# Performance work log

Measured on AMD Instinct MI355X. Metric: run time of the kernel, lower is better.

The kernel has to match this reference:

```python
import jax, jax.numpy as jnp
import numpy as np

K_LAYERS = 10
ALPHA = 0.1
N_NODES = 100000
N_EDGES = 500000
N_PATHS = 3
D = 128
HID = 128


def setup_inputs() -> dict:
    key = jax.random.key(0)
    k1, k2, k3, k4 = jax.random.split(key, 4)
    h = jax.random.normal(k1, (N_NODES, D), dtype=jnp.float32)
    edges = jax.random.randint(k2, (N_PATHS, 2, N_EDGES), 0, N_NODES, dtype=jnp.int64)
    W1 = jax.random.normal(k3, (D, HID), dtype=jnp.float32) * (1.0 / np.sqrt(D))
    b1 = jnp.zeros((HID,), dtype=jnp.float32)
    w2 = jax.random.normal(k4, (HID, 1), dtype=jnp.float32) * (1.0 / np.sqrt(HID))
    return {"h": h, "edges": edges, "W1": W1, "b1": b1, "w2": w2}


def _appnp(h0, src, dst):
    # DGL APPNPConv (eval mode, no dropout): symmetric degree normalization,
    # K steps of h <- (1-alpha) * D_in^{-1/2} A D_out^{-1/2} h + alpha * h0
    n = h0.shape[0]
    ones = jnp.ones(src.shape[0], dtype=h0.dtype)
    out_deg = jnp.clip(jax.ops.segment_sum(ones, src, num_segments=n), 1.0)
    in_deg = jnp.clip(jax.ops.segment_sum(ones, dst, num_segments=n), 1.0)
    norm_s = out_deg ** -0.5  # [N]
    norm_d = in_deg ** -0.5   # [N]

    def step(x, _):
        msg = (x * norm_s[:, None])[src]                       # [E, D] gather
        agg = jax.ops.segment_sum(msg, dst, num_segments=n)    # [N, D] scatter-add
        x = (1.0 - ALPHA) * (agg * norm_d[:, None]) + ALPHA * h0
        return x, None

    x, _ = jax.lax.scan(step, h0, None, length=K_LAYERS)
    return x


def reference(h, edges, W1, b1, w2):
    src = edges[:, 0, :]  # [P, E]
    dst = edges[:, 1, :]
    # one APPNP propagation per meta-path, vmapped over the P axis
    z = jax.vmap(lambda s, d: _appnp(h, s, d))(src, dst)  # [P, N, D]
    z = jnp.transpose(z, (1, 0, 2))                        # [N, P, D]
    # semantic attention: small MLP -> mean over nodes -> softmax over paths
    w = jnp.tanh(z @ W1 + b1) @ w2   # [N, P, 1]
    w = w.mean(axis=0)               # [P, 1]
    beta = jax.nn.softmax(w, axis=0) # [P, 1]
    return (beta[None, :, :] * z).sum(axis=1)  # [N, D]
```

## Files before the change

kernel.cpp:

```cpp
#include <hip/hip_runtime.h>
#include <math.h>

#define N_NODES 100000
#define N_EDGES 500000
#define N_PATHS 3
#define DIM 128
#define K_LAYERS 10
#define NBLK_PER_PATH ((N_NODES + 255) / 256)
#define PN (N_PATHS * N_NODES)
#define HRANGE 16384
#define NRANGE ((N_NODES + HRANGE - 1) / HRANGE)
#define BPG 8

typedef __attribute__((ext_vector_type(8))) short bf16x8;
typedef __attribute__((ext_vector_type(4))) float f32x4;

__device__ __forceinline__ float bflo(unsigned u) { return __uint_as_float(u << 16); }
__device__ __forceinline__ float bfhi(unsigned u) { return __uint_as_float(u & 0xffff0000u); }

__global__ __launch_bounds__(256) void hist_kernel(const int* __restrict__ edges,
                                                   int* __restrict__ partial) {
    __shared__ int hist[HRANGE];
    int g = blockIdx.x / BPG;
    int b = blockIdx.x - g * BPG;
    int r = g % NRANGE;
    int pt = g / NRANGE;
    int p = pt >> 1, t = pt & 1;
    for (int i = threadIdx.x; i < HRANGE; i += 256) hist[i] = 0;
    __syncthreads();
    const int* arr = edges + ((size_t)p * 2 + t) * N_EDGES;
    int lo = r * HRANGE;
    const int chunk = N_EDGES / BPG;
    int beg = b * chunk;
    for (int i = beg + threadIdx.x; i < beg + chunk; i += 256) {
        int v = arr[i] - lo;
        if ((unsigned)v < HRANGE) atomicAdd(&hist[v], 1);
    }
    __syncthreads();
    int* outp = partial + ((size_t)g * BPG + b) * HRANGE;
    for (int i = threadIdx.x; i < HRANGE; i += 256) outp[i] = hist[i];
}

__global__ __launch_bounds__(256) void deg_reduce_kernel(const int* __restrict__ partial,
                                                         float* __restrict__ norm_s,
                                                         float* __restrict__ norm_d,
                                                         int* __restrict__ degD_tot) {
    int i = blockIdx.x * 256 + threadIdx.x;
    if (i >= PN) return;
    int p = i / N_NODES, n = i - p * N_NODES;
    int r = n / HRANGE, off = n - r * HRANGE;
    const int* ps = partial + (((size_t)(p * 2 + 0) * NRANGE + r) * BPG) * HRANGE + off;
    const int* pd = partial + (((size_t)(p * 2 + 1) * NRANGE + r) * BPG) * HRANGE + off;
    int sS = 0, sD = 0;
#pragma unroll
    for (int b = 0; b < BPG; ++b) {
        sS += ps[(size_t)b * HRANGE];
        sD += pd[(size_t)b * HRANGE];
    }
    norm_s[i] = 1.0f / sqrtf(fmaxf((float)sS, 1.0f));
    norm_d[i] = 1.0f / sqrtf(fmaxf((float)sD, 1.0f));
    degD_tot[i] = sD;
}

__global__ __launch_bounds__(256) void blocksum_kernel(const int* __restrict__ cnt,
                                                       int* __restrict__ bsum) {
    int b = blockIdx.x;
    int p = b / NBLK_PER_PATH;
    int lb = b - p * NBLK_PER_PATH;
    int idx = lb * 256 + threadIdx.x;
    int v = (idx < N_NODES) ? cnt[p * N_NODES + idx] : 0;
#pragma unroll
    for (int off = 32; off; off >>= 1) v += __shfl_xor(v, off);
    __shared__ int ws[4];
    if ((threadIdx.x & 63) == 0) ws[threadIdx.x >> 6] = v;
    __syncthreads();
    if (threadIdx.x == 0) bsum[b] = ws[0] + ws[1] + ws[2] + ws[3];
}

__global__ __launch_bounds__(512) void bscan_kernel(int* __restrict__ bsum) {
    __shared__ int s[512];
    int p = blockIdx.x;
    int t = threadIdx.x;
    int v = (t < NBLK_PER_PATH) ? bsum[p * NBLK_PER_PATH + t] : 0;
    s[t] = v;
    __syncthreads();
    for (int off = 1; off < 512; off <<= 1) {
        int x = s[t];
        int a = (t >= off) ? s[t - off] : 0;
        __syncthreads();
        s[t] = x + a;
        __syncthreads();
    }
    if (t < NBLK_PER_PATH) bsum[p * NBLK_PER_PATH + t] = s[t] - v;
}

__global__ __launch_bounds__(256) void scan_write_kernel(const int* __restrict__ cnt,
                                                         const int* __restrict__ bsum,
                                                         int* __restrict__ row_ptr_all,
                                                         int* __restrict__ cursor_all) {
    __shared__ int s[256];
    int b = blockIdx.x;
    int p = b / NBLK_PER_PATH;
    int lb = b - p * NBLK_PER_PATH;
    int idx = lb * 256 + threadIdx.x;
    int t = threadIdx.x;
    int v = (idx < N_NODES) ? cnt[p * N_NODES + idx] : 0;
    s[t] = v;
    __syncthreads();
    for (int off = 1; off < 256; off <<= 1) {
        int x = s[t];
        int a = (t >= off) ? s[t - off] : 0;
        __syncthreads();
        s[t] = x + a;
        __syncthreads();
    }
    int excl = s[t] - v + bsum[b];
    if (idx < N_NODES) {
        row_ptr_all[p * (N_NODES + 1) + idx] = excl;
        cursor_all[p * N_NODES + idx] = excl;
        if (idx == N_NODES - 1)
            row_ptr_all[p * (N_NODES + 1) + N_NODES] = excl + v;
    }
}

__global__ __launch_bounds__(256) void fill_kernel(const int* __restrict__ edges,
                                                   const float* __restrict__ norm_s,
                                                   const float* __restrict__ norm_d,
                                                   int* __restrict__ cursor,
                                                   int2* __restrict__ cw) {
    int idx = blockIdx.x * 256 + threadIdx.x;
    if (idx < N_PATHS * N_EDGES) {
        int p = idx / N_EDGES;
        int e = idx - p * N_EDGES;
        const int* src = edges + (size_t)p * 2 * N_EDGES;
        const int* dst = src + N_EDGES;
        int s = src[e], d = dst[e];
        int pos = atomicAdd(&cursor[p * N_NODES + d], 1);
        float w = 0.9f * norm_s[p * N_NODES + s] * norm_d[p * N_NODES + d];
        cw[(size_t)p * N_EDGES + pos] = make_int2(s, __float_as_int(w));
    }
}

__device__ __forceinline__ unsigned bf16pack(float a, float b) {
    unsigned ua = __float_as_uint(a), ub = __float_as_uint(b);
    ua = (ua + 0x7fffu + ((ua >> 16) & 1)) >> 16;
    ub = (ub + 0x7fffu + ((ub >> 16) & 1)) >> 16;
    return ua | (ub << 16);
}

__global__ __launch_bounds__(256) void cast_kernel(const float4* __restrict__ in,
                                                   ushort4* __restrict__ outp) {
    int idx = blockIdx.x * 256 + threadIdx.x;
    if (idx < N_NODES * DIM / 4) {
        float4 v = in[idx];
        ushort4 o;
        unsigned u;
        u = __float_as_uint(v.x); o.x = (unsigned short)((u + 0x7fff + ((u >> 16) & 1)) >> 16);
        u = __float_as_uint(v.y); o.y = (unsigned short)((u + 0x7fff + ((u >> 16) & 1)) >> 16);
        u = __float_as_uint(v.z); o.z = (unsigned short)((u + 0x7fff + ((u >> 16) & 1)) >> 16);
        u = __float_as_uint(v.w); o.w = (unsigned short)((u + 0x7fff + ((u >> 16) & 1)) >> 16);
        outp[idx] = o;
    }
}

__global__ __launch_bounds__(256) void w1t_kernel(const float* __restrict__ W1,
                                                  unsigned short* __restrict__ W1t) {
    int idx = blockIdx.x * 256 + threadIdx.x;
    if (idx < DIM * DIM) {
        int c = idx >> 7, k = idx & 127;
        unsigned u = __float_as_uint(W1[k * DIM + c]);
        W1t[idx] = (unsigned short)((u + 0x7fff + ((u >> 16) & 1)) >> 16);
    }
}

template <int OUT_F32, int H_BF16>
__global__ __launch_bounds__(256) void prop_kernel(const unsigned short* __restrict__ xin,
                                                   size_t in_stride,
                                                   const void* __restrict__ anchor,
                                                   void* __restrict__ xout,
                                                   const int* __restrict__ row_ptr,
                                                   const int2* __restrict__ cw) {
    int wid  = threadIdx.x >> 6;
    int lane = threadIdx.x & 63;
    int q    = lane >> 4;
    int ql   = lane & 15;
    int nodeBase = blockIdx.x * 16 + wid * 4;
    int p  = nodeBase / N_NODES;
    int nb = nodeBase - p * N_NODES;
    const int*  rp   = row_ptr + p * (N_NODES + 1);
    const int2* cwp  = cw + (size_t)p * N_EDGES;
    const uint4* xin4 = (const uint4*)(xin + (size_t)p * in_stride);

    int rv = 0;
    if (lane < 5) rv = rp[nb + lane];
    int beg = __shfl(rv, q);
    int end = __shfl(rv, q + 1);
    int deg = end - beg;
    int myNode = nb + q;
    int maxd = deg;
    maxd = max(maxd, __shfl_xor(maxd, 16));
    maxd = max(maxd, __shfl_xor(maxd, 32));

    float a0 = 0.f, a1 = 0.f, a2 = 0.f, a3 = 0.f;
    float a4 = 0.f, a5 = 0.f, a6 = 0.f, a7 = 0.f;

    for (int base = 0; base < maxd; base += 16) {
        int2 e = make_int2(0, 0);
        if (base + ql < deg) e = cwp[beg + base + ql];
        int lim = maxd - base; if (lim > 16) lim = 16;
#pragma unroll 4
        for (int j = 0; j < lim; ++j) {
            int lsrc = (lane & 48) | j;
            int   c = __shfl(e.x, lsrc);
            float w = __int_as_float(__shfl(e.y, lsrc));
            if (base + j < deg) {
                uint4 v = xin4[(size_t)c * 16 + ql];
                a0 = fmaf(w, bflo(v.x), a0);
                a1 = fmaf(w, bfhi(v.x), a1);
                a2 = fmaf(w, bflo(v.y), a2);
                a3 = fmaf(w, bfhi(v.y), a3);
                a4 = fmaf(w, bflo(v.z), a4);
                a5 = fmaf(w, bfhi(v.z), a5);
                a6 = fmaf(w, bflo(v.w), a6);
                a7 = fmaf(w, bfhi(v.w), a7);
            }
        }
    }

    if (H_BF16) {
        uint4 hv = ((const uint4*)anchor)[(size_t)myNode * 16 + ql];
        a0 += 0.1f * bflo(hv.x); a1 += 0.1f * bfhi(hv.x);
        a2 += 0.1f * bflo(hv.y); a3 += 0.1f * bfhi(hv.y);
        a4 += 0.1f * bflo(hv.z); a5 += 0.1f * bfhi(hv.z);
        a6 += 0.1f * bflo(hv.w); a7 += 0.1f * bfhi(hv.w);
    } else {
        const float4* h4 = (const float4*)anchor + (size_t)myNode * 32;
        float4 h0v = h4[ql * 2];
        float4 h1v = h4[ql * 2 + 1];
        a0 += 0.1f * h0v.x; a1 += 0.1f * h0v.y; a2 += 0.1f * h0v.z; a3 += 0.1f * h0v.w;
        a4 += 0.1f * h1v.x; a5 += 0.1f * h1v.y; a6 += 0.1f * h1v.z; a7 += 0.1f * h1v.w;
    }

    size_t row = (size_t)p * N_NODES + myNode;
    if (OUT_F32) {
        float4* zo = (float4*)xout + row * 32;
        zo[ql * 2]     = make_float4(a0, a1, a2, a3);
        zo[ql * 2 + 1] = make_float4(a4, a5, a6, a7);
    } else {
        uint4 o;
        o.x = bf16pack(a0, a1);
        o.y = bf16pack(a2, a3);
        o.z = bf16pack(a4, a5);
        o.w = bf16pack(a6, a7);
        ((uint4*)xout)[row * 16 + ql] = o;
    }
}

__device__ __forceinline__ float fast_tanh(float x) {
    float e = __expf(2.0f * x);
    return 1.0f - 2.0f / (e + 1.0f);
}

__global__ __launch_bounds__(256) void attn_kernel(const float* __restrict__ z,
                                                   const unsigned short* __restrict__ W1t,
                                                   const float* __restrict__ b1,
                                                   const float* __restrict__ w2,
                                                   float* __restrict__ wsum) {
    const int wid  = threadIdx.x >> 6;
    const int lane = threadIdx.x & 63;
    const int c0   = lane & 15;
    const int kh   = lane >> 4;

    const bf16x8* w1t8 = (const bf16x8*)W1t;
    bf16x8 Bf[8][4];
#pragma unroll
    for (int nt = 0; nt < 8; ++nt)
#pragma unroll
        for (int ks = 0; ks < 4; ++ks)
            Bf[nt][ks] = w1t8[(nt * 16 + c0) * 16 + ks * 4 + kh];

    float b1v[8], w2v[8];
#pragma unroll
    for (int nt = 0; nt < 8; ++nt) {
        b1v[nt] = b1[nt * 16 + c0];
        w2v[nt] = w2[nt * 16 + c0];
    }

    float accP0 = 0.f, accP1 = 0.f, accP2 = 0.f;
    const int NTILES = N_PATHS * N_NODES / 16;
    const int TPP    = N_NODES / 16;
    const int stride = gridDim.x * 4;
    const float4* zf4 = (const float4*)z;

    for (int t = blockIdx.x * 4 + wid; t < NTILES; t += stride) {
        size_t rbase = ((size_t)t * 16 + c0) * 32 + kh * 2;
        bf16x8 Af[4];
#pragma unroll
        for (int ks = 0; ks < 4; ++ks) {
            float4 x0 = zf4[rbase + ks * 8];
            float4 x1 = zf4[rbase + ks * 8 + 1];
            union { uint4 u; bf16x8 v; } cv;
            cv.u.x = bf16pack(x0.x, x0.y);
            cv.u.y = bf16pack(x0.z, x0.w);
            cv.u.z = bf16pack(x1.x, x1.y);
            cv.u.w = bf16pack(x1.z, x1.w);
            Af[ks] = cv.v;
        }
        f32x4 acc[8];
#pragma unroll
        for (int nt = 0; nt < 8; ++nt) acc[nt] = (f32x4){0.f, 0.f, 0.f, 0.f};
#pragma unroll
        for (int nt = 0; nt < 8; ++nt)
#pragma unroll
            for (int ks = 0; ks < 4; ++ks)
                acc[nt] = __builtin_amdgcn_mfma_f32_16x16x32_bf16(Af[ks], Bf[nt][ks], acc[nt], 0, 0, 0);

        float psum = 0.f;
#pragma unroll
        for (int nt = 0; nt < 8; ++nt) {
            psum += fast_tanh(acc[nt][0] + b1v[nt]) * w2v[nt];
            psum += fast_tanh(acc[nt][1] + b1v[nt]) * w2v[nt];
            psum += fast_tanh(acc[nt][2] + b1v[nt]) * w2v[nt];
            psum += fast_tanh(acc[nt][3] + b1v[nt]) * w2v[nt];
        }
#pragma unroll
        for (int off = 32; off; off >>= 1) psum += __shfl_xor(psum, off);
        if (lane == 0) {
            int p = t / TPP;
            if (p == 0) accP0 += psum;
            else if (p == 1) accP1 += psum;
            else accP2 += psum;
        }
    }
    if (lane == 0) {
        if (accP0 != 0.f) atomicAdd(&wsum[0], accP0);
        if (accP1 != 0.f) atomicAdd(&wsum[1], accP1);
        if (accP2 != 0.f) atomicAdd(&wsum[2], accP2);
    }
}

__global__ void beta_kernel(const float* __restrict__ wsum, float* __restrict__ beta) {
    if (threadIdx.x == 0 && blockIdx.x == 0) {
        float w0 = wsum[0] * (1.0f / N_NODES);
        float w1 = wsum[1] * (1.0f / N_NODES);
        float w2v = wsum[2] * (1.0f / N_NODES);
        float m = fmaxf(w0, fmaxf(w1, w2v));
        float e0 = expf(w0 - m), e1 = expf(w1 - m), e2 = expf(w2v - m);
        float inv = 1.0f / (e0 + e1 + e2);
        beta[0] = e0 * inv;
        beta[1] = e1 * inv;
        beta[2] = e2 * inv;
    }
}

__global__ __launch_bounds__(256) void combine_kernel(const float4* __restrict__ z4,
                                                      const float* __restrict__ beta,
                                                      float4* __restrict__ out4) {
    size_t idx = (size_t)blockIdx.x * 256 + threadIdx.x;
    const size_t M = (size_t)N_NODES * 32;
    if (idx < M) {
        float b0 = beta[0], b1 = beta[1], b2 = beta[2];
        float4 a = z4[idx];
        float4 b = z4[M + idx];
        float4 c = z4[2 * M + idx];
        float4 o;
        o.x = b0 * a.x + b1 * b.x + b2 * c.x;
        o.y = b0 * a.y + b1 * b.y + b2 * c.y;
        o.z = b0 * a.z + b1 * b.z + b2 * c.z;
        o.w = b0 * a.w + b1 * b.w + b2 * c.w;
        out4[idx] = o;
    }
}

extern "C" void kernel_launch(void* const* d_in, const int* in_sizes, int n_in,
                              void* d_out, int out_size, void* d_ws, size_t ws_size,
                              hipStream_t stream) {
    const float* h     = (const float*)d_in[0];
    const int*   edges = (const int*)d_in[1];
    const float* W1    = (const float*)d_in[2];
    const float* b1    = (const float*)d_in[3];
    const float* w2    = (const float*)d_in[4];
    float* out = (float*)d_out;

    char* ws = (char*)d_ws;
    float* z = (float*)ws;               ws += (size_t)N_PATHS * N_NODES * DIM * 4;
    unsigned short* buf0 = (unsigned short*)ws; ws += (size_t)N_PATHS * N_NODES * DIM * 2;
    int2* cw = (int2*)ws;                ws += (size_t)N_PATHS * N_EDGES * 8;
    int* row_ptr = (int*)ws;             ws += (size_t)N_PATHS * (N_NODES + 1) * 4 + 12;
    float* norm_s = (float*)ws;          ws += (size_t)PN * 4;
    float* norm_d = (float*)ws;          ws += (size_t)PN * 4;
    int* bsum = (int*)ws;                ws += (size_t)N_PATHS * NBLK_PER_PATH * 4;
    float* wsum = (float*)ws;            ws += 4 * 4;
    float* beta = (float*)ws;            ws += 4 * 4;
    unsigned short* W1t = (unsigned short*)ws; ws += (size_t)DIM * DIM * 2;
    int* partial  = (int*)buf0;
    int* degD_tot = partial + (size_t)3 * 2 * NRANGE * BPG * HRANGE;
    int* cursor   = degD_tot + PN;
    unsigned short* buf1 = (unsigned short*)z;
    unsigned short* hb   = (unsigned short*)z + (size_t)N_PATHS * N_NODES * DIM;

    const size_t PSTRIDE = (size_t)N_NODES * DIM;

    hist_kernel<<<3 * 2 * NRANGE * BPG, 256, 0, stream>>>(edges, partial);
    deg_reduce_kernel<<<(PN + 255) / 256, 256, 0, stream>>>(partial, norm_s, norm_d, degD_tot);
    blocksum_kernel<<<N_PATHS * NBLK_PER_PATH, 256, 0, stream>>>(degD_tot, bsum);
    bscan_kernel<<<N_PATHS, 512, 0, stream>>>(bsum);
    scan_write_kernel<<<N_PATHS * NBLK_PER_PATH, 256, 0, stream>>>(degD_tot, bsum, row_ptr, cursor);
    fill_kernel<<<(N_PATHS * N_EDGES + 255) / 256, 256, 0, stream>>>(edges, norm_s, norm_d, cursor, cw);

    cast_kernel<<<(N_NODES * DIM / 4 + 255) / 256, 256, 0, stream>>>(
        (const float4*)h, (ushort4*)hb);
    w1t_kernel<<<(DIM * DIM + 255) / 256, 256, 0, stream>>>(W1, W1t);

    const int pgrid = N_PATHS * N_NODES / 16;
    prop_kernel<0, 1><<<pgrid, 256, 0, stream>>>(hb, 0, hb, buf0, row_ptr, cw);
    for (int i = 1; i <= 8; ++i) {
        const unsigned short* src_b = (i & 1) ? buf0 : buf1;
        unsigned short* dst_b       = (i & 1) ? buf1 : buf0;
        prop_kernel<0, 1><<<pgrid, 256, 0, stream>>>(src_b, PSTRIDE, hb, dst_b, row_ptr, cw);
    }
    prop_kernel<1, 0><<<pgrid, 256, 0, stream>>>(buf0, PSTRIDE, h, z, row_ptr, cw);

    hipMemsetAsync(wsum, 0, 3 * 4, stream);
    attn_kernel<<<512, 256, 0, stream>>>(z, W1t, b1, w2, wsum);
    beta_kernel<<<1, 64, 0, stream>>>(wsum, beta);
    combine_kernel<<<(N_NODES * 32 + 255) / 256, 256, 0, stream>>>(
        (const float4*)z, beta, (float4*)out);
}
```

Baseline: 1.110 ms.

## Process eight nodes per wavefront with 16 features per lane in propagation

Propagation now assigns 8 lanes per node (8 nodes per wave, 32 per block), each lane loading two 16-byte chunks and keeping 16 accumulators instead of 8, with edges fetched in batches of 8. This halves the lanes per gather and the per-node shuffle overhead, and doubles memory-level parallelism per lane. Divergence from degree imbalance rises because more nodes share a wave's max-degree loop. The degree histogram is also retuned to smaller shared-memory ranges with more blocks per group.

New measurement: 1.119 ms. Within noise of the previous version (+0.8%).

```diff
diff --git a/kernel.cpp b/kernel.cpp
--- a/kernel.cpp
+++ b/kernel.cpp
@@ -8,9 +8,9 @@
 #define K_LAYERS 10
 #define NBLK_PER_PATH ((N_NODES + 255) / 256)
 #define PN (N_PATHS * N_NODES)
-#define HRANGE 16384
+#define HRANGE 8192
 #define NRANGE ((N_NODES + HRANGE - 1) / HRANGE)
-#define BPG 8
+#define BPG 16
 
 typedef __attribute__((ext_vector_type(8))) short bf16x8;
 typedef __attribute__((ext_vector_type(4))) float f32x4;
@@ -182,9 +182,9 @@
                                                    const int2* __restrict__ cw) {
     int wid  = threadIdx.x >> 6;
     int lane = threadIdx.x & 63;
-    int q    = lane >> 4;
-    int ql   = lane & 15;
-    int nodeBase = blockIdx.x * 16 + wid * 4;
+    int oct  = lane >> 3;
+    int ol   = lane & 7;
+    int nodeBase = blockIdx.x * 32 + wid * 8;
     int p  = nodeBase / N_NODES;
     int nb = nodeBase - p * N_NODES;
     const int*  rp   = row_ptr + p * (N_NODES + 1);
@@ -192,67 +192,81 @@
     const uint4* xin4 = (const uint4*)(xin + (size_t)p * in_stride);
 
     int rv = 0;
-    if (lane < 5) rv = rp[nb + lane];
-    int beg = __shfl(rv, q);
-    int end = __shfl(rv, q + 1);
+    if (lane < 9) rv = rp[nb + lane];
+    int beg = __shfl(rv, oct);
+    int end = __shfl(rv, oct + 1);
     int deg = end - beg;
-    int myNode = nb + q;
+    int myNode = nb + oct;
     int maxd = deg;
+    maxd = max(maxd, __shfl_xor(maxd, 8));
     maxd = max(maxd, __shfl_xor(maxd, 16));
     maxd = max(maxd, __shfl_xor(maxd, 32));
 
     float a0 = 0.f, a1 = 0.f, a2 = 0.f, a3 = 0.f;
     float a4 = 0.f, a5 = 0.f, a6 = 0.f, a7 = 0.f;
-
-    for (int base = 0; base < maxd; base += 16) {
+    float a8 = 0.f, a9 = 0.f, a10 = 0.f, a11 = 0.f;
+    float a12 = 0.f, a13 = 0.f, a14 = 0.f, a15 = 0.f;
+
+    for (int base = 0; base < maxd; base += 8) {
         int2 e = make_int2(0, 0);
-        if (base + ql < deg) e = cwp[beg + base + ql];
-        int lim = maxd - base; if (lim > 16) lim = 16;
+        if (base + ol < deg) e = cwp[beg + base + ol];
+        int lim = maxd - base; if (lim > 8) lim = 8;
 #pragma unroll 4
         for (int j = 0; j < lim; ++j) {
-            int lsrc = (lane & 48) | j;
+            int lsrc = (lane & 56) | j;
             int   c = __shfl(e.x, lsrc);
             float w = __int_as_float(__shfl(e.y, lsrc));
             if (base + j < deg) {
-                uint4 v = xin4[(size_t)c * 16 + ql];
-                a0 = fmaf(w, bflo(v.x), a0);
-                a1 = fmaf(w, bfhi(v.x), a1);
-                a2 = fmaf(w, bflo(v.y), a2);
-                a3 = fmaf(w, bfhi(v.y), a3);
-                a4 = fmaf(w, bflo(v.z), a4);
-                a5 = fmaf(w, bfhi(v.z), a5);
-                a6 = fmaf(w, bflo(v.w), a6);
-                a7 = fmaf(w, bfhi(v.w), a7);
+                uint4 v1 = xin4[(size_t)c * 16 + ol];
+                uint4 v2 = xin4[(size_t)c * 16 + 8 + ol];
+                a0  = fmaf(w, bflo(v1.x), a0);  a1  = fmaf(w, bfhi(v1.x), a1);
+                a2  = fmaf(w, bflo(v1.y), a2);  a3  = fmaf(w, bfhi(v1.y), a3);
+                a4  = fmaf(w, bflo(v1.z), a4);  a5  = fmaf(w, bfhi(v1.z), a5);
+                a6  = fmaf(w, bflo(v1.w), a6);  a7  = fmaf(w, bfhi(v1.w), a7);
+                a8  = fmaf(w, bflo(v2.x), a8);  a9  = fmaf(w, bfhi(v2.x), a9);
+                a10 = fmaf(w, bflo(v2.y), a10); a11 = fmaf(w, bfhi(v2.y), a11);
+                a12 = fmaf(w, bflo(v2.z), a12); a13 = fmaf(w, bfhi(v2.z), a13);
+                a14 = fmaf(w, bflo(v2.w), a14); a15 = fmaf(w, bfhi(v2.w), a15);
             }
         }
     }
 
     if (H_BF16) {
-        uint4 hv = ((const uint4*)anchor)[(size_t)myNode * 16 + ql];
-        a0 += 0.1f * bflo(hv.x); a1 += 0.1f * bfhi(hv.x);
-        a2 += 0.1f * bflo(hv.y); a3 += 0.1f * bfhi(hv.y);
-        a4 += 0.1f * bflo(hv.z); a5 += 0.1f * bfhi(hv.z);
-        a6 += 0.1f * bflo(hv.w); a7 += 0.1f * bfhi(hv.w);
+        uint4 hv1 = ((const uint4*)anchor)[(size_t)myNode * 16 + ol];
+        uint4 hv2 = ((const uint4*)anchor)[(size_t)myNode * 16 + 8 + ol];
+        a0  += 0.1f * bflo(hv1.x); a1  += 0.1f * bfhi(hv1.x);
+        a2  += 0.1f * bflo(hv1.y); a3  += 0.1f * bfhi(hv1.y);
+        a4  += 0.1f * bflo(hv1.z); a5  += 0.1f * bfhi(hv1.z);
+        a6  += 0.1f * bflo(hv1.w); a7  += 0.1f * bfhi(hv1.w);
+        a8  += 0.1f * bflo(hv2.x); a9  += 0.1f * bfhi(hv2.x);
+        a10 += 0.1f * bflo(hv2.y); a11 += 0.1f * bfhi(hv2.y);
+        a12 += 0.1f * bflo(hv2.z); a13 += 0.1f * bfhi(hv2.z);
+        a14 += 0.1f * bflo(hv2.w); a15 += 0.1f * bfhi(hv2.w);
     } else {
         const float4* h4 = (const float4*)anchor + (size_t)myNode * 32;
-        float4 h0v = h4[ql * 2];
-        float4 h1v = h4[ql * 2 + 1];
-        a0 += 0.1f * h0v.x; a1 += 0.1f * h0v.y; a2 += 0.1f * h0v.z; a3 += 0.1f * h0v.w;
-        a4 += 0.1f * h1v.x; a5 += 0.1f * h1v.y; a6 += 0.1f * h1v.z; a7 += 0.1f * h1v.w;
+        float4 p0 = h4[ol * 2], p1 = h4[ol * 2 + 1];
+        float4 p2 = h4[ol * 2 + 16], p3 = h4[ol * 2 + 17];
+        a0  += 0.1f * p0.x; a1  += 0.1f * p0.y; a2  += 0.1f * p0.z; a3  += 0.1f * p0.w;
+        a4  += 0.1f * p1.x; a5  += 0.1f * p1.y; a6  += 0.1f * p1.z; a7  += 0.1f * p1.w;
+        a8  += 0.1f * p2.x; a9  += 0.1f * p2.y; a10 += 0.1f * p2.z; a11 += 0.1f * p2.w;
+        a12 += 0.1f * p3.x; a13 += 0.1f * p3.y; a14 += 0.1f * p3.z; a15 += 0.1f * p3.w;
     }
 
     size_t row = (size_t)p * N_NODES + myNode;
     if (OUT_F32) {
         float4* zo = (float4*)xout + row * 32;
-        zo[ql * 2]     = make_float4(a0, a1, a2, a3);
-        zo[ql * 2 + 1] = make_float4(a4, a5, a6, a7);
+        zo[ol * 2]      = make_float4(a0, a1, a2, a3);
+        zo[ol * 2 + 1]  = make_float4(a4, a5, a6, a7);
+        zo[ol * 2 + 16] = make_float4(a8, a9, a10, a11);
+        zo[ol * 2 + 17] = make_float4(a12, a13, a14, a15);
     } else {
-        uint4 o;
-        o.x = bf16pack(a0, a1);
-        o.y = bf16pack(a2, a3);
-        o.z = bf16pack(a4, a5);
-        o.w = bf16pack(a6, a7);
-        ((uint4*)xout)[row * 16 + ql] = o;
+        uint4 o1, o2;
+        o1.x = bf16pack(a0, a1);   o1.y = bf16pack(a2, a3);
+        o1.z = bf16pack(a4, a5);   o1.w = bf16pack(a6, a7);
+        o2.x = bf16pack(a8, a9);   o2.y = bf16pack(a10, a11);
+        o2.z = bf16pack(a12, a13); o2.w = bf16pack(a14, a15);
+        ((uint4*)xout)[row * 16 + ol]     = o1;
+        ((uint4*)xout)[row * 16 + 8 + ol] = o2;
     }
 }
 
@@ -412,7 +426,7 @@
         (const float4*)h, (ushort4*)hb);
     w1t_kernel<<<(DIM * DIM + 255) / 256, 256, 0, stream>>>(W1, W1t);
 
-    const int pgrid = N_PATHS * N_NODES / 16;
+    const int pgrid = PN / 32;
     prop_kernel<0, 1><<<pgrid, 256, 0, stream>>>(hb, 0, hb, buf0, row_ptr, cw);
     for (int i = 1; i <= 8; ++i) {
         const unsigned short* src_b = (i & 1) ? buf0 : buf1;
```
